# Optimization experiments

Measured on AMD Instinct MI355X. Metric: run time of the kernel, lower is better.

## Reference

```python
import jax, jax.numpy as jnp
import numpy as np

B = 64; H = 64; W = 64; C = 128
NH = 4; WS = 4; SHIFT = 2
N = WS * WS; HD = C // NH; SCALE = HD ** -0.5
HID = 4 * C; EPS = 1e-6


def _rel_index():
    # faithful to source: meshgrid(coords_w, coords_h, indexing='ij'); hard-coded 4 == WS
    coords = np.stack(np.meshgrid(np.arange(WS), np.arange(WS), indexing='ij')).reshape(2, -1)
    rel = coords[:, :, None] - coords[:, None, :]
    rel = rel.transpose(1, 2, 0).copy()
    rel[:, :, 0] += WS - 1
    rel[:, :, 1] += WS - 1
    rel[:, :, 0] *= 2 * WS - 1
    return rel.sum(-1)  # (N, N) int

REL_IDX = jnp.asarray(_rel_index())


def _attn_mask():
    img = np.zeros((H, W))
    sl = (slice(0, -WS), slice(-WS, -SHIFT), slice(-SHIFT, None))
    cnt = 0
    for hs in sl:
        for ws_ in sl:
            img[hs, ws_] = cnt
            cnt += 1
    mw = img.reshape(H // WS, WS, W // WS, WS).transpose(0, 2, 1, 3).reshape(-1, N)
    m = mw[:, None, :] - mw[:, :, None]  # (nW, N, N)
    return jnp.asarray(np.where(m != 0, -100.0, 0.0).astype(np.float32))

MASK = _attn_mask()  # (nW, N, N)


def _ln(x, s, b):
    mu = x.mean(-1, keepdims=True)
    var = ((x - mu) ** 2).mean(-1, keepdims=True)
    return (x - mu) * jax.lax.rsqrt(var + EPS) * s + b


def setup_inputs() -> dict:
    key = jax.random.key(0)
    ks = jax.random.split(key, 8)
    def nrm(k, shape, scale=0.02):
        return jax.random.normal(k, shape, jnp.float32) * scale
    return dict(
        x=jax.random.normal(ks[0], (B, H * W, C), jnp.float32),
        ln1_scale=jnp.ones((C,), jnp.float32), ln1_bias=jnp.zeros((C,), jnp.float32),
        qkv_w=nrm(ks[1], (C, 3 * C)), qkv_b=jnp.zeros((3 * C,), jnp.float32),
        rel_bias=nrm(ks[2], ((2 * WS - 1) ** 2, NH)),
        proj_w=nrm(ks[3], (C, C)), proj_b=jnp.zeros((C,), jnp.float32),
        ln2_scale=jnp.ones((C,), jnp.float32), ln2_bias=jnp.zeros((C,), jnp.float32),
        fc1_w=nrm(ks[4], (C, HID)), fc1_b=jnp.zeros((HID,), jnp.float32),
        fc2_w=nrm(ks[5], (HID, C)), fc2_b=jnp.zeros((C,), jnp.float32),
    )


def reference(x, ln1_scale, ln1_bias, qkv_w, qkv_b, rel_bias, proj_w, proj_b,
              ln2_scale, ln2_bias, fc1_w, fc1_b, fc2_w, fc2_b):
    shortcut = x
    h = _ln(x, ln1_scale, ln1_bias).reshape(B, H, W, C)
    h = jnp.roll(h, (-SHIFT, -SHIFT), axis=(1, 2))
    # window partition -> (B*nW, N, C)
    xw = h.reshape(B, H // WS, WS, W // WS, WS, C).transpose(0, 1, 3, 2, 4, 5).reshape(-1, N, C)
    B_ = xw.shape[0]
    qkv = (xw @ qkv_w + qkv_b).reshape(B_, N, 3, NH, HD).transpose(2, 0, 3, 1, 4)
    q, k, v = qkv[0] * SCALE, qkv[1], qkv[2]
    attn = jnp.einsum('bhnd,bhmd->bhnm', q, k)  # (B_, NH, N, N)
    bias = rel_bias[REL_IDX.reshape(-1)].reshape(N, N, NH).transpose(2, 0, 1)
    attn = attn + bias[None]
    nW = MASK.shape[0]
    attn = attn.reshape(B_ // nW, nW, NH, N, N) + MASK[None, :, None]
    attn = jax.nn.softmax(attn.reshape(B_, NH, N, N), axis=-1)
    attn = jax.nn.softmax(attn, axis=-1)  # source applies softmax twice when mask is present
    out = jnp.einsum('bhnm,bhmd->bhnd', attn, v).transpose(0, 2, 1, 3).reshape(B_, N, C)
    out = out @ proj_w + proj_b
    # window reverse
    h = out.reshape(B, H // WS, W // WS, WS, WS, C).transpose(0, 1, 3, 2, 4, 5).reshape(B, H, W, C)
    h = jnp.roll(h, (SHIFT, SHIFT), axis=(1, 2)).reshape(B, H * W, C)
    x = shortcut + h
    m = _ln(x, ln2_scale, ln2_bias)
    m = jax.nn.gelu(m @ fc1_w + fc1_b) @ fc2_w + fc2_b  # flax nn.gelu default approximate=True
    return x + m
```

## Files before the change

### kernel.cpp

```cpp
#include <hip/hip_runtime.h>

typedef __bf16 bf16x8 __attribute__((ext_vector_type(8)));
typedef __bf16 bf16x4 __attribute__((ext_vector_type(4)));
typedef float f32x4 __attribute__((ext_vector_type(4)));
typedef unsigned short us8 __attribute__((ext_vector_type(8)));
typedef unsigned short us4 __attribute__((ext_vector_type(4)));
typedef short sh4 __attribute__((ext_vector_type(4)));

#define SCALE_Q 0.17677669529663687f

__device__ __forceinline__ unsigned short f2b(float f) {
    __bf16 h = (__bf16)f;
    return __builtin_bit_cast(unsigned short, h);
}
__device__ __forceinline__ float b2f(unsigned short h) {
    union { unsigned u; float f; } v; v.u = ((unsigned)h) << 16;
    return v.f;
}
__device__ __forceinline__ f32x4 mfma16(us8 a, us8 b, f32x4 c) {
    return __builtin_amdgcn_mfma_f32_16x16x32_bf16(
        __builtin_bit_cast(bf16x8, a), __builtin_bit_cast(bf16x8, b), c, 0, 0, 0);
}

#if __has_builtin(__builtin_amdgcn_mfma_f32_16x16x16bf16_1k)
__device__ __forceinline__ f32x4 mfma16k16(us4 a, us4 b, f32x4 c) {
    return __builtin_amdgcn_mfma_f32_16x16x16bf16_1k(
        __builtin_bit_cast(sh4, a), __builtin_bit_cast(sh4, b), c, 0, 0, 0);
}
#elif __has_builtin(__builtin_amdgcn_mfma_f32_16x16x16_bf16)
__device__ __forceinline__ f32x4 mfma16k16(us4 a, us4 b, f32x4 c) {
    return __builtin_amdgcn_mfma_f32_16x16x16_bf16(
        __builtin_bit_cast(bf16x4, a), __builtin_bit_cast(bf16x4, b), c, 0, 0, 0);
}
#else
__device__ __forceinline__ f32x4 mfma16k16(us4 a, us4 b, f32x4 c) {
    asm volatile("v_mfma_f32_16x16x16_bf16 %0, %1, %2, %0"
                 : "+v"(c) : "v"(a), "v"(b));
    return c;
}
#endif

__device__ __forceinline__ us8 lds_ld8(const unsigned short* base, int byteoff) {
    return *(const us8*)((const char*)base + byteoff);
}
__device__ __forceinline__ void lds_st8(unsigned short* base, int byteoff, us8 v) {
    *(us8*)((char*)base + byteoff) = v;
}

__global__ void k_pack_qkvw(const float* __restrict__ qkv_w, unsigned short* __restrict__ dst) {
    int gid = blockIdx.x * 256 + threadIdx.x;
    int blk = gid >> 9, rem = gid & 511;
    int lane = rem >> 3, j = rem & 7;
    int w = blk / 24, r1 = blk % 24, ct = r1 >> 2, kk = r1 & 3;
    int col = w * 96 + ct * 16 + (lane & 15);
    int k = kk * 32 + (lane >> 4) * 8 + j;
    float v = qkv_w[k * 384 + col];
    if (col < 128) v *= SCALE_Q;
    dst[gid] = f2b(v);
}
__global__ void k_scale_qkvb(const float* __restrict__ qkv_b, float* __restrict__ dst) {
    int i = blockIdx.x * 256 + threadIdx.x;
    if (i < 384) dst[i] = qkv_b[i] * (i < 128 ? SCALE_Q : 1.f);
}
__global__ void k_pack_projw(const float* __restrict__ proj_w, unsigned short* __restrict__ dst) {
    int gid = blockIdx.x * 256 + threadIdx.x;
    int blk = gid >> 9, rem = gid & 511;
    int lane = rem >> 3, j = rem & 7;
    int w = blk >> 3, r1 = blk & 7, ct = r1 >> 2, kk = r1 & 3;
    int col = w * 32 + ct * 16 + (lane & 15);
    int k = kk * 32 + (lane >> 4) * 8 + j;
    dst[gid] = f2b(proj_w[k * 128 + col]);
}

__global__ void k_pack_mlp(const float* __restrict__ fc1_w, const float* __restrict__ fc2_w,
                           unsigned short* __restrict__ wPack) {
    int gid = blockIdx.x * 256 + threadIdx.x;
    int ct = gid >> 12;
    int byte = (gid & 4095) * 2;
    float v;
    if (byte < 4096) {
        int kk = byte >> 10, rem = byte & 1023;
        int lane = rem >> 4, j = (rem & 15) >> 1;
        v = fc1_w[(size_t)(kk * 32 + (lane >> 4) * 8 + j) * 512 + ct * 16 + (lane & 15)];
    } else {
        int b2 = byte - 4096;
        int co = b2 >> 9, rem = b2 & 511;
        int lane = rem >> 3, j = (rem & 7) >> 1;
        v = fc2_w[(size_t)(ct * 16 + (lane >> 4) * 4 + j) * 128 + co * 16 + (lane & 15)];
    }
    wPack[gid] = f2b(v);
}

__global__ __launch_bounds__(256, 3) void k_block1(
    const float* __restrict__ x,
    const float* __restrict__ ln1s, const float* __restrict__ ln1b,
    const unsigned short* __restrict__ qkvWp, const float* __restrict__ qkvBs,
    const float* __restrict__ relb,
    const unsigned short* __restrict__ projWp, const float* __restrict__ projB,
    float* __restrict__ out)
{
    __shared__ unsigned short sm[4 * 6144];
    __shared__ float sbias[196];
    const int tid = threadIdx.x;
    const int wave = tid >> 6, lane = tid & 63;
    const int g = lane >> 4, m16 = lane & 15;
    if (tid < 196) sbias[tid] = relb[tid];
    const int win0 = blockIdx.x * 4;
    const int winM = win0 + wave;
    const int bbM = winM >> 8, whM = (winM >> 4) & 15, wnM = winM & 15;

    {
        float4 sc0 = *(const float4*)(ln1s + m16 * 8);
        float4 sc1 = *(const float4*)(ln1s + m16 * 8 + 4);
        float4 bi0 = *(const float4*)(ln1b + m16 * 8);
        float4 bi1 = *(const float4*)(ln1b + m16 * 8 + 4);
        #pragma unroll
        for (int it = 0; it < 4; ++it) {
            int tok = it * 4 + g;
            int ti = tok >> 2, tj = tok & 3;
            int hh = (whM * 4 + ti + 2) & 63, ww = (wnM * 4 + tj + 2) & 63;
            const float* xr = x + ((((size_t)bbM << 12) | (hh << 6) | ww) * 128) + m16 * 8;
            float4 v0 = *(const float4*)xr, v1 = *(const float4*)(xr + 4);
            float sum = v0.x + v0.y + v0.z + v0.w + v1.x + v1.y + v1.z + v1.w;
            float sq  = v0.x*v0.x + v0.y*v0.y + v0.z*v0.z + v0.w*v0.w
                      + v1.x*v1.x + v1.y*v1.y + v1.z*v1.z + v1.w*v1.w;
            #pragma unroll
            for (int m = 1; m < 16; m <<= 1) { sum += __shfl_xor(sum, m); sq += __shfl_xor(sq, m); }
            float mu = sum * 0.0078125f;
            float rstd = rsqrtf(sq * 0.0078125f - mu * mu + 1e-6f);
            us8 o;
            o[0] = f2b((v0.x - mu) * rstd * sc0.x + bi0.x);
            o[1] = f2b((v0.y - mu) * rstd * sc0.y + bi0.y);
            o[2] = f2b((v0.z - mu) * rstd * sc0.z + bi0.z);
            o[3] = f2b((v0.w - mu) * rstd * sc0.w + bi0.w);
            o[4] = f2b((v1.x - mu) * rstd * sc1.x + bi1.x);
            o[5] = f2b((v1.y - mu) * rstd * sc1.y + bi1.y);
            o[6] = f2b((v1.z - mu) * rstd * sc1.z + bi1.z);
            o[7] = f2b((v1.w - mu) * rstd * sc1.w + bi1.w);
            lds_st8(sm, wave * 12288 + tok * 256 + ((m16 * 16) ^ ((tok & 7) << 4)), o);
        }
    }
    __syncthreads();

    us8 afr[4][4];
    #pragma unroll
    for (int w = 0; w < 4; ++w)
        #pragma unroll
        for (int k = 0; k < 4; ++k)
            afr[w][k] = lds_ld8(sm, w * 12288 + m16 * 256 + ((k * 64 + g * 16) ^ ((m16 & 7) << 4)));
    __syncthreads();

    #pragma unroll
    for (int ct = 0; ct < 6; ++ct) {
        const unsigned short* bp = qkvWp + (size_t)((wave * 6 + ct) * 4) * 512 + lane * 8;
        us8 b0 = *(const us8*)(bp);
        us8 b1 = *(const us8*)(bp + 512);
        us8 b2 = *(const us8*)(bp + 1024);
        us8 b3 = *(const us8*)(bp + 1536);
        f32x4 acc[4] = {{0.f,0.f,0.f,0.f},{0.f,0.f,0.f,0.f},{0.f,0.f,0.f,0.f},{0.f,0.f,0.f,0.f}};
        #pragma unroll
        for (int w = 0; w < 4; ++w) {
            acc[w] = mfma16(afr[w][0], b0, acc[w]);
            acc[w] = mfma16(afr[w][1], b1, acc[w]);
            acc[w] = mfma16(afr[w][2], b2, acc[w]);
            acc[w] = mfma16(afr[w][3], b3, acc[w]);
        }
        const int c = wave * 96 + ct * 16 + m16;
        const float bias = qkvBs[c];
        const int s = c >> 7;
        const int rem = c & 127, hq = rem >> 5, hd = rem & 31;
        #pragma unroll
        for (int w = 0; w < 4; ++w) {
            const int base = w * 12288;
            if (s == 2) {
                us4 pk;
                #pragma unroll
                for (int jj = 0; jj < 4; ++jj) pk[jj] = f2b(acc[w][jj] + bias);
                *(us4*)((char*)sm + base + 8192 + hq * 1024 + hd * 32
                        + ((g ^ ((hd >> 2) & 3)) << 3)) = pk;
            } else {
                #pragma unroll
                for (int jj = 0; jj < 4; ++jj) {
                    int tok = g * 4 + jj;
                    int chunk = (hd >> 3) ^ ((tok >> 1) & 3);
                    *(unsigned short*)((char*)sm + base + s * 4096 + hq * 1024
                                       + tok * 64 + chunk * 16 + (hd & 7) * 2)
                        = f2b(acc[w][jj] + bias);
                }
            }
        }
    }
    __syncthreads();

    {
        const int base = wave * 12288;
        const int ti = m16 >> 2, tj = m16 & 3;
        const int hhq = whM * 4 + ti, wwq = wnM * 4 + tj;
        const int myid = (hhq < 60 ? 0 : (hhq < 62 ? 3 : 6)) + (wwq < 60 ? 0 : (wwq < 62 ? 1 : 2));
        const int qkswz = (g ^ ((m16 >> 1) & 3)) * 16;
        const int vswz  = (g ^ ((m16 >> 2) & 3)) << 3;
        f32x4 po[4][2];
        #pragma unroll
        for (int h = 0; h < 4; ++h) {
            us8 kf = lds_ld8(sm, base + 4096 + h * 1024 + m16 * 64 + qkswz);
            us8 qf = lds_ld8(sm, base +        h * 1024 + m16 * 64 + qkswz);
            f32x4 st = mfma16(kf, qf, (f32x4){0.f,0.f,0.f,0.f});
            float p[4];
            #pragma unroll
            for (int jj = 0; jj < 4; ++jj) {
                int kk = g * 4 + jj;
                int pi = kk >> 2, pj = kk & 3;
                int hhk = whM * 4 + pi, wwk = wnM * 4 + pj;
                int pid = (hhk < 60 ? 0 : (hhk < 62 ? 3 : 6)) + (wwk < 60 ? 0 : (wwk < 62 ? 1 : 2));
                float v = st[jj] + sbias[((ti - pi + 3) * 7 + (tj - pj + 3)) * 4 + h];
                p[jj] = (pid != myid) ? v - 100.f : v;
            }
            #pragma unroll
            for (int rep = 0; rep < 2; ++rep) {
                float mx = fmaxf(fmaxf(p[0], p[1]), fmaxf(p[2], p[3]));
                mx = fmaxf(mx, __shfl_xor(mx, 16));
                mx = fmaxf(mx, __shfl_xor(mx, 32));
                float ssum = 0.f;
                #pragma unroll
                for (int jj = 0; jj < 4; ++jj) { p[jj] = __expf(p[jj] - mx); ssum += p[jj]; }
                ssum += __shfl_xor(ssum, 16);
                ssum += __shfl_xor(ssum, 32);
                float inv = 1.f / ssum;
                #pragma unroll
                for (int jj = 0; jj < 4; ++jj) p[jj] *= inv;
            }
            us4 pf;
            #pragma unroll
            for (int jj = 0; jj < 4; ++jj) pf[jj] = f2b(p[jj]);
            #pragma unroll
            for (int dh = 0; dh < 2; ++dh) {
                us4 vf = *(const us4*)((const char*)sm + base + 8192 + h * 1024
                                       + (dh * 16 + m16) * 32 + vswz);
                po[h][dh] = mfma16k16(vf, pf, (f32x4){0.f,0.f,0.f,0.f});
            }
        }
        #pragma unroll
        for (int h = 0; h < 4; ++h)
            #pragma unroll
            for (int dh = 0; dh < 2; ++dh) {
                us4 pk;
                #pragma unroll
                for (int jj = 0; jj < 4; ++jj) pk[jj] = f2b(po[h][dh][jj]);
                *(us4*)((char*)sm + base + m16 * 256
                        + ((h * 64 + dh * 32 + g * 8) ^ ((m16 & 7) << 4))) = pk;
            }
    }
    __syncthreads();

    {
        us8 cfr[4][4];
        #pragma unroll
        for (int w = 0; w < 4; ++w)
            #pragma unroll
            for (int k = 0; k < 4; ++k)
                cfr[w][k] = lds_ld8(sm, w * 12288 + m16 * 256 + ((k * 64 + g * 16) ^ ((m16 & 7) << 4)));
        #pragma unroll
        for (int ct = 0; ct < 2; ++ct) {
            const unsigned short* bp = projWp + (size_t)((wave * 2 + ct) * 4) * 512 + lane * 8;
            us8 b0 = *(const us8*)(bp);
            us8 b1 = *(const us8*)(bp + 512);
            us8 b2 = *(const us8*)(bp + 1024);
            us8 b3 = *(const us8*)(bp + 1536);
            const int c = wave * 32 + ct * 16 + m16;
            const float pb = projB[c];
            #pragma unroll
            for (int w = 0; w < 4; ++w) {
                f32x4 acc = {0.f, 0.f, 0.f, 0.f};
                acc = mfma16(cfr[w][0], b0, acc);
                acc = mfma16(cfr[w][1], b1, acc);
                acc = mfma16(cfr[w][2], b2, acc);
                acc = mfma16(cfr[w][3], b3, acc);
                const int winw = win0 + w;
                const int bb = winw >> 8, wh = (winw >> 4) & 15, wn = winw & 15;
                #pragma unroll
                for (int jj = 0; jj < 4; ++jj) {
                    int tok = g * 4 + jj;
                    int hh3 = (wh * 4 + (tok >> 2) + 2) & 63;
                    int ww3 = (wn * 4 + (tok & 3) + 2) & 63;
                    size_t t = (((size_t)bb << 12) | (hh3 << 6) | ww3);
                    out[t * 128 + c] = acc[jj] + pb + x[t * 128 + c];
                }
            }
        }
    }
}

__global__ __launch_bounds__(512, 4) void k_block2(
    float* __restrict__ out,
    const float* __restrict__ ln2s, const float* __restrict__ ln2b,
    const unsigned short* __restrict__ wPack,
    const float* __restrict__ fc1B, const float* __restrict__ fc2B)
{
    __shared__ unsigned short scratch[8][2048];
    __shared__ unsigned short wbuf[2][4096];
    const int tid = threadIdx.x;
    const int wave = tid >> 6, lane = tid & 63;
    const int g = lane >> 4, m16 = lane & 15;
    const size_t r0 = (size_t)blockIdx.x * 128;

    {
        const unsigned short* src = wPack + tid * 8;
        unsigned short* dst = &wbuf[0][wave * 512];
#if __has_builtin(__builtin_amdgcn_global_load_lds)
        __builtin_amdgcn_global_load_lds(
            (const __attribute__((address_space(1))) void*)src,
            (__attribute__((address_space(3))) void*)dst, 16, 0, 0);
#else
        *(us8*)(dst + lane * 8) = *(const us8*)src;
#endif
    }

    {
        float4 sc0 = *(const float4*)(ln2s + m16 * 8);
        float4 sc1 = *(const float4*)(ln2s + m16 * 8 + 4);
        float4 bi0 = *(const float4*)(ln2b + m16 * 8);
        float4 bi1 = *(const float4*)(ln2b + m16 * 8 + 4);
        #pragma unroll
        for (int it = 0; it < 4; ++it) {
            int lr = it * 4 + g;
            const float* xr = out + (r0 + wave * 16 + lr) * 128 + m16 * 8;
            float4 v0 = *(const float4*)xr, v1 = *(const float4*)(xr + 4);
            float sum = v0.x + v0.y + v0.z + v0.w + v1.x + v1.y + v1.z + v1.w;
            float sq  = v0.x*v0.x + v0.y*v0.y + v0.z*v0.z + v0.w*v0.w
                      + v1.x*v1.x + v1.y*v1.y + v1.z*v1.z + v1.w*v1.w;
            #pragma unroll
            for (int m = 1; m < 16; m <<= 1) { sum += __shfl_xor(sum, m); sq += __shfl_xor(sq, m); }
            float mu = sum * 0.0078125f;
            float rstd = rsqrtf(sq * 0.0078125f - mu * mu + 1e-6f);
            us8 o;
            o[0] = f2b((v0.x - mu) * rstd * sc0.x + bi0.x);
            o[1] = f2b((v0.y - mu) * rstd * sc0.y + bi0.y);
            o[2] = f2b((v0.z - mu) * rstd * sc0.z + bi0.z);
            o[3] = f2b((v0.w - mu) * rstd * sc0.w + bi0.w);
            o[4] = f2b((v1.x - mu) * rstd * sc1.x + bi1.x);
            o[5] = f2b((v1.y - mu) * rstd * sc1.y + bi1.y);
            o[6] = f2b((v1.z - mu) * rstd * sc1.z + bi1.z);
            o[7] = f2b((v1.w - mu) * rstd * sc1.w + bi1.w);
            lds_st8(&scratch[wave][0], lr * 256 + ((m16 * 16) ^ ((lr & 7) << 4)), o);
        }
    }

    us8 bx[4];
    #pragma unroll
    for (int kk = 0; kk < 4; ++kk)
        bx[kk] = lds_ld8(&scratch[wave][0],
                         m16 * 256 + ((kk * 64 + g * 16) ^ ((m16 & 7) << 4)));
    __syncthreads();

    f32x4 accO[8];
    #pragma unroll
    for (int co = 0; co < 8; ++co) accO[co] = (f32x4){0.f, 0.f, 0.f, 0.f};

    for (int ct = 0; ct < 32; ++ct) {
        if (ct < 31) {
            const unsigned short* src = wPack + (ct + 1) * 4096 + tid * 8;
            unsigned short* dst = &wbuf[(ct + 1) & 1][wave * 512];
#if __has_builtin(__builtin_amdgcn_global_load_lds)
            __builtin_amdgcn_global_load_lds(
                (const __attribute__((address_space(1))) void*)src,
                (__attribute__((address_space(3))) void*)dst, 16, 0, 0);
#else
            *(us8*)(dst + lane * 8) = *(const us8*)src;
#endif
        }
        const char* wb = (const char*)&wbuf[ct & 1][0];
        us8 aw0 = *(const us8*)(wb + 0 * 1024 + lane * 16);
        us8 aw1 = *(const us8*)(wb + 1 * 1024 + lane * 16);
        us8 aw2 = *(const us8*)(wb + 2 * 1024 + lane * 16);
        us8 aw3 = *(const us8*)(wb + 3 * 1024 + lane * 16);
        f32x4 h = {0.f, 0.f, 0.f, 0.f};
        h = mfma16(aw0, bx[0], h);
        h = mfma16(aw1, bx[1], h);
        h = mfma16(aw2, bx[2], h);
        h = mfma16(aw3, bx[3], h);
        float4 b1v = *(const float4*)(fc1B + ct * 16 + g * 4);
        us4 pa;
        #pragma unroll
        for (int jj = 0; jj < 4; ++jj) {
            float v = h[jj] + ((const float*)&b1v)[jj];
            float z = v + 0.044715f * v * v * v;
            float e = __builtin_amdgcn_exp2f(-2.3022082f * z);
            pa[jj] = f2b(v * __builtin_amdgcn_rcpf(1.f + e));
        }
        #pragma unroll
        for (int co = 0; co < 8; ++co) {
            us4 bw = *(const us4*)(wb + 4096 + co * 512 + lane * 8);
            accO[co] = mfma16k16(pa, bw, accO[co]);
        }
        __syncthreads();
    }

    #pragma unroll
    for (int co = 0; co < 8; ++co) {
        int col = co * 16 + m16;
        float b2v = fc2B[col];
        #pragma unroll
        for (int jj = 0; jj < 4; ++jj) {
            size_t row = r0 + wave * 16 + g * 4 + jj;
            float* op = out + row * 128 + col;
            *op = accO[co][jj] + b2v + *op;
        }
    }
}

extern "C" void kernel_launch(void* const* d_in, const int* in_sizes, int n_in,
                              void* d_out, int out_size, void* d_ws, size_t ws_size,
                              hipStream_t stream) {
    const float* x        = (const float*)d_in[0];
    const float* ln1_s    = (const float*)d_in[1];
    const float* ln1_b    = (const float*)d_in[2];
    const float* qkv_w    = (const float*)d_in[3];
    const float* qkv_b    = (const float*)d_in[4];
    const float* rel_bias = (const float*)d_in[5];
    const float* proj_w   = (const float*)d_in[6];
    const float* proj_b   = (const float*)d_in[7];
    const float* ln2_s    = (const float*)d_in[8];
    const float* ln2_b    = (const float*)d_in[9];
    const float* fc1_w    = (const float*)d_in[10];
    const float* fc1_b    = (const float*)d_in[11];
    const float* fc2_w    = (const float*)d_in[12];
    const float* fc2_b    = (const float*)d_in[13];
    float* out = (float*)d_out;
    char* ws = (char*)d_ws;

    unsigned short* qkv_wp  = (unsigned short*)(ws);
    unsigned short* proj_wp = (unsigned short*)(ws + 98304);
    unsigned short* wpack   = (unsigned short*)(ws + 131072);
    float*          qkv_bs  = (float*)(ws + 393216);

    k_pack_qkvw<<<192, 256, 0, stream>>>(qkv_w, qkv_wp);
    k_scale_qkvb<<<2, 256, 0, stream>>>(qkv_b, qkv_bs);
    k_pack_projw<<<64, 256, 0, stream>>>(proj_w, proj_wp);
    k_pack_mlp<<<512, 256, 0, stream>>>(fc1_w, fc2_w, wpack);

    k_block1<<<4096, 256, 0, stream>>>(x, ln1_s, ln1_b, qkv_wp, qkv_bs, rel_bias,
                                       proj_wp, proj_b, out);
    k_block2<<<2048, 512, 0, stream>>>(out, ln2_s, ln2_b, wpack, fc1_b, fc2_b);
}
```

Baseline: 233.1 us.

## Pair hidden tiles in MLP to use K=32 MFMA for fc2

Reorganises the packed MLP weights so two 16-column fc1 tiles are processed per iteration, with the columns interleaved so the GELU outputs form an 8-wide K=32 operand for fc2. This replaces the 16x16x16 MFMAs in fc2 with 16x16x32 ones and halves the number of loop iterations and barriers. It also reuses the LDS scratch area for the weight double buffer, so the first weight prefetch now starts only after the layernorm stage instead of overlapping it.

```diff
diff --git a/kernel.cpp b/kernel.cpp
--- a/kernel.cpp
+++ b/kernel.cpp
@@ -75,18 +75,24 @@
 __global__ void k_pack_mlp(const float* __restrict__ fc1_w, const float* __restrict__ fc2_w,
                            unsigned short* __restrict__ wPack) {
     int gid = blockIdx.x * 256 + threadIdx.x;
-    int ct = gid >> 12;
-    int byte = (gid & 4095) * 2;
+    int pair = gid >> 13;
+    int rem = gid & 8191;
     float v;
-    if (byte < 4096) {
-        int kk = byte >> 10, rem = byte & 1023;
-        int lane = rem >> 4, j = (rem & 15) >> 1;
-        v = fc1_w[(size_t)(kk * 32 + (lane >> 4) * 8 + j) * 512 + ct * 16 + (lane & 15)];
+    if (rem < 4096) {
+        int half = rem >> 11;
+        int r2 = rem & 2047;
+        int kk = r2 >> 9, r3 = r2 & 511;
+        int lane = r3 >> 3, j = r3 & 7;
+        int m = lane & 15;
+        int col = pair * 32 + (m >> 2) * 8 + half * 4 + (m & 3);
+        int k = kk * 32 + (lane >> 4) * 8 + j;
+        v = fc1_w[(size_t)k * 512 + col];
     } else {
-        int b2 = byte - 4096;
-        int co = b2 >> 9, rem = b2 & 511;
-        int lane = rem >> 3, j = (rem & 7) >> 1;
-        v = fc2_w[(size_t)(ct * 16 + (lane >> 4) * 4 + j) * 128 + co * 16 + (lane & 15)];
+        int r2 = rem - 4096;
+        int co = r2 >> 9, r3 = r2 & 511;
+        int lane = r3 >> 3, j = r3 & 7;
+        int k = pair * 32 + (lane >> 4) * 8 + j;
+        v = fc2_w[(size_t)k * 128 + co * 16 + (lane & 15)];
     }
     wPack[gid] = f2b(v);
 }
@@ -296,24 +302,12 @@
     const unsigned short* __restrict__ wPack,
     const float* __restrict__ fc1B, const float* __restrict__ fc2B)
 {
-    __shared__ unsigned short scratch[8][2048];
-    __shared__ unsigned short wbuf[2][4096];
+    __shared__ unsigned short smem[16384];
     const int tid = threadIdx.x;
     const int wave = tid >> 6, lane = tid & 63;
     const int g = lane >> 4, m16 = lane & 15;
     const size_t r0 = (size_t)blockIdx.x * 128;
-
-    {
-        const unsigned short* src = wPack + tid * 8;
-        unsigned short* dst = &wbuf[0][wave * 512];
-#if __has_builtin(__builtin_amdgcn_global_load_lds)
-        __builtin_amdgcn_global_load_lds(
-            (const __attribute__((address_space(1))) void*)src,
-            (__attribute__((address_space(3))) void*)dst, 16, 0, 0);
-#else
-        *(us8*)(dst + lane * 8) = *(const us8*)src;
-#endif
-    }
+    unsigned short* scr = &smem[wave * 2048];
 
     {
         float4 sc0 = *(const float4*)(ln2s + m16 * 8);
@@ -341,56 +335,77 @@
             o[5] = f2b((v1.y - mu) * rstd * sc1.y + bi1.y);
             o[6] = f2b((v1.z - mu) * rstd * sc1.z + bi1.z);
             o[7] = f2b((v1.w - mu) * rstd * sc1.w + bi1.w);
-            lds_st8(&scratch[wave][0], lr * 256 + ((m16 * 16) ^ ((lr & 7) << 4)), o);
-        }
-    }
-
+            lds_st8(scr, lr * 256 + ((m16 * 16) ^ ((lr & 7) << 4)), o);
+        }
+    }
     us8 bx[4];
     #pragma unroll
     for (int kk = 0; kk < 4; ++kk)
-        bx[kk] = lds_ld8(&scratch[wave][0],
-                         m16 * 256 + ((kk * 64 + g * 16) ^ ((m16 & 7) << 4)));
+        bx[kk] = lds_ld8(scr, m16 * 256 + ((kk * 64 + g * 16) ^ ((m16 & 7) << 4)));
+    __syncthreads();
+
+    #pragma unroll
+    for (int sub = 0; sub < 2; ++sub) {
+        const unsigned short* src = wPack + sub * 4096 + tid * 8;
+        unsigned short* dst = &smem[sub * 4096 + wave * 512];
+#if __has_builtin(__builtin_amdgcn_global_load_lds)
+        __builtin_amdgcn_global_load_lds(
+            (const __attribute__((address_space(1))) void*)src,
+            (__attribute__((address_space(3))) void*)dst, 16, 0, 0);
+#else
+        *(us8*)(dst + lane * 8) = *(const us8*)src;
+#endif
+    }
     __syncthreads();
 
     f32x4 accO[8];
     #pragma unroll
     for (int co = 0; co < 8; ++co) accO[co] = (f32x4){0.f, 0.f, 0.f, 0.f};
 
-    for (int ct = 0; ct < 32; ++ct) {
-        if (ct < 31) {
-            const unsigned short* src = wPack + (ct + 1) * 4096 + tid * 8;
-            unsigned short* dst = &wbuf[(ct + 1) & 1][wave * 512];
+    for (int p = 0; p < 16; ++p) {
+        if (p < 15) {
+            #pragma unroll
+            for (int sub = 0; sub < 2; ++sub) {
+                const unsigned short* src = wPack + (p + 1) * 8192 + sub * 4096 + tid * 8;
+                unsigned short* dst = &smem[((p + 1) & 1) * 8192 + sub * 4096 + wave * 512];
 #if __has_builtin(__builtin_amdgcn_global_load_lds)
-            __builtin_amdgcn_global_load_lds(
-                (const __attribute__((address_space(1))) void*)src,
-                (__attribute__((address_space(3))) void*)dst, 16, 0, 0);
+                __builtin_amdgcn_global_load_lds(
+                    (const __attribute__((address_space(1))) void*)src,
+                    (__attribute__((address_space(3))) void*)dst, 16, 0, 0);
 #else
-            *(us8*)(dst + lane * 8) = *(const us8*)src;
+                *(us8*)(dst + lane * 8) = *(const us8*)src;
 #endif
-        }
-        const char* wb = (const char*)&wbuf[ct & 1][0];
-        us8 aw0 = *(const us8*)(wb + 0 * 1024 + lane * 16);
-        us8 aw1 = *(const us8*)(wb + 1 * 1024 + lane * 16);
-        us8 aw2 = *(const us8*)(wb + 2 * 1024 + lane * 16);
-        us8 aw3 = *(const us8*)(wb + 3 * 1024 + lane * 16);
-        f32x4 h = {0.f, 0.f, 0.f, 0.f};
-        h = mfma16(aw0, bx[0], h);
-        h = mfma16(aw1, bx[1], h);
-        h = mfma16(aw2, bx[2], h);
-        h = mfma16(aw3, bx[3], h);
-        float4 b1v = *(const float4*)(fc1B + ct * 16 + g * 4);
-        us4 pa;
+            }
+        }
+        const char* wb = (const char*)&smem[(p & 1) * 8192];
+        f32x4 hA = {0.f, 0.f, 0.f, 0.f};
+        hA = mfma16(*(const us8*)(wb +    0 + lane * 16), bx[0], hA);
+        hA = mfma16(*(const us8*)(wb + 1024 + lane * 16), bx[1], hA);
+        hA = mfma16(*(const us8*)(wb + 2048 + lane * 16), bx[2], hA);
+        hA = mfma16(*(const us8*)(wb + 3072 + lane * 16), bx[3], hA);
+        f32x4 hB = {0.f, 0.f, 0.f, 0.f};
+        hB = mfma16(*(const us8*)(wb + 4096 + lane * 16), bx[0], hB);
+        hB = mfma16(*(const us8*)(wb + 5120 + lane * 16), bx[1], hB);
+        hB = mfma16(*(const us8*)(wb + 6144 + lane * 16), bx[2], hB);
+        hB = mfma16(*(const us8*)(wb + 7168 + lane * 16), bx[3], hB);
+        float4 bA = *(const float4*)(fc1B + p * 32 + g * 8);
+        float4 bB = *(const float4*)(fc1B + p * 32 + g * 8 + 4);
+        us8 pa;
         #pragma unroll
         for (int jj = 0; jj < 4; ++jj) {
-            float v = h[jj] + ((const float*)&b1v)[jj];
+            float v = hA[jj] + ((const float*)&bA)[jj];
             float z = v + 0.044715f * v * v * v;
             float e = __builtin_amdgcn_exp2f(-2.3022082f * z);
             pa[jj] = f2b(v * __builtin_amdgcn_rcpf(1.f + e));
+            float w = hB[jj] + ((const float*)&bB)[jj];
+            float z2 = w + 0.044715f * w * w * w;
+            float e2 = __builtin_amdgcn_exp2f(-2.3022082f * z2);
+            pa[4 + jj] = f2b(w * __builtin_amdgcn_rcpf(1.f + e2));
         }
         #pragma unroll
         for (int co = 0; co < 8; ++co) {
-            us4 bw = *(const us4*)(wb + 4096 + co * 512 + lane * 8);
-            accO[co] = mfma16k16(pa, bw, accO[co]);
+            us8 bw = *(const us8*)(wb + 8192 + co * 1024 + lane * 16);
+            accO[co] = mfma16(pa, bw, accO[co]);
         }
         __syncthreads();
     }
```

After: 223.5 us. 4.1% less time.
